# Performance work log

Measured on AMD Instinct MI355X. Metric: run time of the kernel, lower is better.

Reference implementation:

```python
import jax, jax.numpy as jnp
import numpy as np

N_AE = 64
N_GRAPHS = 4096
N_ELE = 16384
EPS = 1e-5


def _seg_mean(v, idx, num_segments):
    s = jax.ops.segment_sum(v, idx, num_segments=num_segments)
    c = jax.ops.segment_sum(jnp.ones((v.shape[0], 1), v.dtype), idx, num_segments=num_segments)
    return s / jnp.maximum(c, 1.0)


def _batchnorm(h, gamma, beta):
    mu = jnp.mean(h, axis=0)
    var = jnp.mean(jnp.square(h - mu), axis=0)  # biased, as torch BN training fwd
    return (h - mu) * jax.lax.rsqrt(var + EPS) * gamma + beta


def _dist_layer(x, dist_feat, atom_idx, ele_idx, W, b, gamma, beta):
    # x: [N, 2*n_ae]
    pa = jax.nn.relu(_seg_mean(x[:, :N_AE], atom_idx, N_GRAPHS))[atom_idx]   # [N, n_ae]
    pe = jax.nn.relu(_seg_mean(x[:, N_AE:], ele_idx, N_ELE))[ele_idx]        # [N, n_ae]
    h = jnp.concatenate([dist_feat, pa, pe], axis=1)                          # [N, n_de+2*n_ae]
    h = h @ W.T + b                                                           # [N, 2*n_ae]
    h = _batchnorm(h, gamma, beta)
    return jax.nn.relu(h + x)


def setup_inputs() -> dict:
    key = jax.random.key(0)
    ks = jax.random.split(key, 12)
    N = 500000
    n_re = 64
    n_be = 64
    d = 2 * N_AE
    inp = {
        "x": jax.random.normal(ks[0], (N, d), jnp.float32),
        "rdf_feat": jax.random.normal(ks[1], (N, n_re), jnp.float32),
        "bdf_feat": jax.random.normal(ks[2], (N, n_be), jnp.float32),
        "atom_idx": jnp.sort(jax.random.randint(ks[3], (N,), 0, N_GRAPHS)),
        "ele_idx": jax.random.randint(ks[4], (N,), 0, N_ELE),
        "rdf_W": jax.random.normal(ks[5], (d, n_re + d), jnp.float32) * 0.05,
        "rdf_b": jnp.zeros((d,), jnp.float32),
        "rdf_gamma": jnp.ones((d,), jnp.float32),
        "rdf_beta": jnp.zeros((d,), jnp.float32),
        "bdf_W": jax.random.normal(ks[6], (d, n_be + d), jnp.float32) * 0.05,
        "bdf_b": jnp.zeros((d,), jnp.float32),
        "bdf_gamma": jnp.ones((d,), jnp.float32),
        "bdf_beta": jnp.zeros((d,), jnp.float32),
        "fc_W": jax.random.normal(ks[7], (d, 2 * d), jnp.float32) * 0.05,
        "fc_b": jnp.zeros((d,), jnp.float32),
    }
    return inp


def reference(x, rdf_feat, bdf_feat, atom_idx, ele_idx,
              rdf_W, rdf_b, rdf_gamma, rdf_beta,
              bdf_W, bdf_b, bdf_gamma, bdf_beta,
              fc_W, fc_b):
    x1 = _dist_layer(x, rdf_feat, atom_idx, ele_idx, rdf_W, rdf_b, rdf_gamma, rdf_beta)
    x2 = _dist_layer(x, bdf_feat, atom_idx, ele_idx, bdf_W, bdf_b, bdf_gamma, bdf_beta)
    h = jnp.concatenate([x1, x2], axis=1)  # [N, 4*n_ae]
    return jax.nn.relu(h @ fc_W.T + fc_b)  # [N, 2*n_ae]
```

## Files before the change

kernel.cpp:

```cpp
#include <hip/hip_runtime.h>
#include <hip/hip_bf16.h>

#define N_GRAPHS 4096
#define N_ELE 16384
#define EPS 1e-5f

#define A_TAB_OFF 0
#define A_CNT_OFF 262144
#define E_TAB_OFF 266240
#define E_CNT_OFF 1314816
#define STAT_OFF  1331200
#define ZPAD_OFF  1347584
#define ZERO_WORDS 1347588
#define A_TABH_OFF 1347600
#define E_TABH_OFF 1478672
#define W1PK_OFF  2002960
#define FCPK_OFF  2027536
#define SCALE_OFF 2043920
#define SHIFT_OFF 2044176
#define WS_WORDS  2044432

typedef __attribute__((ext_vector_type(8))) short bf16x8;
typedef __attribute__((ext_vector_type(4))) float f32x4;

__device__ __forceinline__ float bf2f(unsigned s) { return __uint_as_float(s << 16); }
__device__ __forceinline__ unsigned f2bf(float f) {
  unsigned u = __float_as_uint(f);
  return (u + 0x7fffu + ((u >> 16) & 1u)) >> 16;
}
__device__ __forceinline__ unsigned pkbf(float a, float b) {
  union { __hip_bfloat16 h; unsigned short u; } ca, cb;
  ca.h = __float2bfloat16(a); cb.h = __float2bfloat16(b);
  return (unsigned)ca.u | ((unsigned)cb.u << 16);
}
__device__ __forceinline__ void gload16(const void* g, void* l) {
  __builtin_amdgcn_global_load_lds(
      (const __attribute__((address_space(1))) unsigned*)g,
      (__attribute__((address_space(3))) unsigned*)l, 16, 0, 0);
}


__global__ void k_prep(const float* __restrict__ W1, const float* __restrict__ W2,
                       const float* __restrict__ fcW, float* __restrict__ ws) {
  int tid = blockIdx.x * 512 + threadIdx.x;
  if (tid < 49152) {
    unsigned short* wpk = (unsigned short*)(ws + W1PK_OFF);
    int L = tid / 24576, rem = tid % 24576;
    int ct = rem / 3072, rem2 = rem % 3072;
    int i = rem2 >> 9, lane = (rem2 >> 3) & 63, j = rem2 & 7;
    int zkb = L ? (i + 2) : (i < 2 ? i : i + 2);
    int zk = zkb * 32 + ((lane >> 4) << 3) + j;
    int kp = L ? (zk - 64) : (zk < 64 ? zk : zk - 64);
    int col = ct * 16 + (lane & 15);
    const float* W = L ? W2 : W1;
    wpk[tid] = (unsigned short)f2bf(W[col * 192 + kp]);
  } else {
    int idx = tid - 49152;
    unsigned short* fpk = (unsigned short*)(ws + FCPK_OFF);
    int ct = idx >> 12, kb = (idx >> 9) & 7, lane = (idx >> 3) & 63, j = idx & 7;
    fpk[idx] = (unsigned short)f2bf(fcW[(ct * 16 + (lane & 15)) * 256 + kb * 32 + ((lane >> 4) << 3) + j]);
  }
}

__global__ void k_seg(const float* __restrict__ x, const int* __restrict__ aidx,
                      const int* __restrict__ eidx, float* __restrict__ ws, int N) {
  float* A_tab = ws + A_TAB_OFF; float* A_cnt = ws + A_CNT_OFF;
  float* E_tab = ws + E_TAB_OFF; float* E_cnt = ws + E_CNT_OFF;
  int t = threadIdx.x;
  int c = t & 63, p = (t >> 6) & 1, s = t >> 7;
  int r0 = blockIdx.x * 256;
  int rend = min(r0 + 256, N);
  if (p == 0) {
    float acc = 0.f, cnt = 0.f; int cur = -1;
    for (int r = r0 + s; r < rend; r += 2) {
      int a = aidx[r];
      float v = x[(size_t)r * 128 + c];
      if (a != cur) {
        if (cur >= 0) { atomicAdd(&A_tab[cur * 64 + c], acc); if (c == 0) atomicAdd(&A_cnt[cur], cnt); }
        cur = a; acc = v; cnt = 1.f;
      } else { acc += v; cnt += 1.f; }
    }
    if (cur >= 0) { atomicAdd(&A_tab[cur * 64 + c], acc); if (c == 0) atomicAdd(&A_cnt[cur], cnt); }
  } else {
    for (int r = r0 + s; r < rend; r += 2) {
      int e = eidx[r];
      float v = x[(size_t)r * 128 + 64 + c];
      atomicAdd(&E_tab[e * 64 + c], v);
      if (c == 0) atomicAdd(&E_cnt[e], 1.f);
    }
  }
}

__global__ void k_fin(float* __restrict__ ws) {
  int i = blockIdx.x * 256 + threadIdx.x;
  unsigned* w32 = (unsigned*)ws;
  if (i < 131072) {
    int e = 2 * i;
    float cnt = fmaxf(ws[A_CNT_OFF + (e >> 6)], 1.f);
    float v0 = fmaxf(ws[A_TAB_OFF + e] / cnt, 0.f);
    float v1 = fmaxf(ws[A_TAB_OFF + e + 1] / cnt, 0.f);
    w32[A_TABH_OFF + i] = f2bf(v0) | (f2bf(v1) << 16);
  }
  if (i < 524288) {
    int e = 2 * i;
    float cnt = fmaxf(ws[E_CNT_OFF + (e >> 6)], 1.f);
    float v0 = fmaxf(ws[E_TAB_OFF + e] / cnt, 0.f);
    float v1 = fmaxf(ws[E_TAB_OFF + e + 1] / cnt, 0.f);
    w32[E_TABH_OFF + i] = f2bf(v0) | (f2bf(v1) << 16);
  }
}

__global__ __launch_bounds__(512) void k_gemm(
    const float* __restrict__ rdf, const float* __restrict__ bdf,
    const int* __restrict__ aidx, const int* __restrict__ eidx,
    float* __restrict__ ws, unsigned* __restrict__ outp, int N) {
  __shared__ __align__(16) char smem[32768];
  const unsigned short* Atabh = (const unsigned short*)(ws + A_TABH_OFF);
  const unsigned short* Etabh = (const unsigned short*)(ws + E_TABH_OFF);
  const void* zpad = (const void*)(ws + ZPAD_OFF);
  int t = threadIdx.x;
  int l = t & 63, w = t >> 6;
  int row0 = blockIdx.x * 64;

  #pragma unroll
  for (int ii = 0; ii < 2; ++ii) {
    int rb = (w * 2 + ii) * 4;
    int r = rb + (l >> 4);
    int srow = row0 + r;
    bool ok = srow < N;
    int s = l & 15;
    int c = (s & 8) | ((s ^ r) & 7);
    const void* src;
    if (c < 8) {
      int ia = ok ? aidx[srow] : 0;
      src = (const void*)(Atabh + ((size_t)ia * 64 + c * 8));
    } else {
      int ie = ok ? eidx[srow] : 0;
      src = (const void*)(Etabh + ((size_t)ie * 64 + (c - 8) * 8));
    }
    if (!ok) src = zpad;
    gload16(src, smem + 16384 + rb * 256);
  }

  {
    int r = t >> 3, c0 = (t & 7) * 2;
    int row = row0 + r;
    bool ok = row < N;
    #pragma unroll
    for (int cc = 0; cc < 2; ++cc) {
      int c = c0 + cc;
      uint4 wv;
      if (ok) {
        const float4* src = (const float4*)(c < 8 ? rdf + (size_t)row * 64 + c * 8
                                                  : bdf + (size_t)row * 64 + (c - 8) * 8);
        float4 f0 = src[0], f1 = src[1];
        wv.x = pkbf(f0.x, f0.y); wv.y = pkbf(f0.z, f0.w);
        wv.z = pkbf(f1.x, f1.y); wv.w = pkbf(f1.z, f1.w);
      } else wv = (uint4){0u, 0u, 0u, 0u};
      int slot = (c & 8) | ((c ^ r) & 7);
      *(uint4*)(smem + r * 256 + slot * 16) = wv;
    }
  }
  __syncthreads();

  int L = w >> 2, ctp = w & 3;
  const unsigned short* WpkL = (const unsigned short*)(ws + W1PK_OFF) + L * 24576;
  f32x4 acc[4][2];
  #pragma unroll
  for (int mt = 0; mt < 4; ++mt)
    #pragma unroll
    for (int cti = 0; cti < 2; ++cti) acc[mt][cti] = (f32x4){0.f, 0.f, 0.f, 0.f};
  int half = l >> 4;
  #pragma unroll
  for (int i = 0; i < 6; ++i) {
    int zkb = L ? (i + 2) : (i < 2 ? i : i + 2);
    int cg = zkb * 4 + half;
    const char* base = smem + (zkb < 4 ? 0 : 16384);
    int cl = cg & 15;
    bf16x8 af[4];
    #pragma unroll
    for (int mt = 0; mt < 4; ++mt) {
      int rr = mt * 16 + (l & 15);
      int slot = (cl & 8) | ((cl ^ rr) & 7);
      af[mt] = *(const bf16x8*)(base + rr * 256 + slot * 16);
    }
    #pragma unroll
    for (int cti = 0; cti < 2; ++cti) {
      bf16x8 bfr = *(const bf16x8*)(WpkL + (((ctp * 2 + cti) * 6 + i) * 64 + l) * 8);
      #pragma unroll
      for (int mt = 0; mt < 4; ++mt)
        acc[mt][cti] = __builtin_amdgcn_mfma_f32_16x16x32_bf16(af[mt], bfr, acc[mt][cti], 0, 0, 0);
    }
  }

  float* stat = ws + STAT_OFF + (blockIdx.x & 31) * 512;
  #pragma unroll
  for (int cti = 0; cti < 2; ++cti) {
    float s = 0.f, q = 0.f;
    #pragma unroll
    for (int mt = 0; mt < 4; ++mt)
      #pragma unroll
      for (int rr = 0; rr < 4; ++rr) { float v = acc[mt][cti][rr]; s += v; q += v * v; }
    s += __shfl_xor(s, 16); s += __shfl_xor(s, 32);
    q += __shfl_xor(q, 16); q += __shfl_xor(q, 32);
    if (l < 16) {
      int gc = L * 128 + ctp * 32 + cti * 16 + l;
      atomicAdd(&stat[gc], s);
      atomicAdd(&stat[256 + gc], q);
    }
  }
  __syncthreads();

  #pragma unroll
  for (int mt = 0; mt < 4; ++mt)
    #pragma unroll
    for (int cti = 0; cti < 2; ++cti)
      #pragma unroll
      for (int rr = 0; rr < 4; ++rr) {
        unsigned ub = pkbf(acc[mt][cti][rr], 0.f) & 0xffffu;
        unsigned pb = (unsigned)__shfl_xor((int)ub, 1);
        if (!(l & 1)) {
          int orow = mt * 16 + ((l >> 4) << 2) + rr;
          int colp = (L * 128 + ctp * 32 + cti * 16 + (l & 15)) >> 1;
          int c = colp >> 2;
          int ec = ((c ^ orow) & 7) | (c & 24);
          *(unsigned*)(smem + orow * 512 + ec * 16 + (colp & 3) * 4) = ub | (pb << 16);
        }
      }
  __syncthreads();
  #pragma unroll
  for (int p = 0; p < 4; ++p) {
    int e = p * 512 + t; int rr = e >> 5, v4 = e & 31;
    int ec = ((v4 ^ rr) & 7) | (v4 & 24);
    uint4 val = *(const uint4*)(smem + rr * 512 + ec * 16);
    if (row0 + rr < N) ((uint4*)outp)[(size_t)(row0 + rr) * 32 + v4] = val;
  }
}

__global__ void k_bnfin(const float* __restrict__ g1, const float* __restrict__ b1,
                        const float* __restrict__ g2, const float* __restrict__ b2,
                        float* __restrict__ ws, int N) {
  int c = threadIdx.x;
  float s = 0.f, q = 0.f;
  for (int m = 0; m < 32; ++m) { s += ws[STAT_OFF + m * 512 + c]; q += ws[STAT_OFF + m * 512 + 256 + c]; }
  float inv = 1.f / (float)N;
  float mu = s * inv;
  float var = fmaxf(q * inv - mu * mu, 0.f);
  int lyr = c >> 7, cc = c & 127;
  float ga = lyr ? g2[cc] : g1[cc];
  float be = lyr ? b2[cc] : b1[cc];
  float sc = ga * rsqrtf(var + EPS);
  ws[SCALE_OFF + c] = sc;
  ws[SHIFT_OFF + c] = be - mu * sc;
}

__global__ __launch_bounds__(512) void k_fc(
    const float* __restrict__ x, const float* __restrict__ fcb,
    float* __restrict__ ws, float* __restrict__ out, int N) {
  __shared__ __align__(16) char smem[32768];
  __shared__ float scsh[512];
  int t = threadIdx.x;
  int l = t & 63, w = t >> 6;
  int r = t >> 3, g = t & 7;
  const unsigned* hp = (const unsigned*)out;
  int row0 = blockIdx.x * 64;
  int row = row0 + r;
  bool ok = row < N;
  uint4 hv[4]; float4 xv[8];
  if (ok) {
    const uint4* hs = (const uint4*)(hp + (size_t)row * 128 + g * 16);
    #pragma unroll
    for (int i = 0; i < 4; ++i) hv[i] = hs[i];
    const float4* xs = (const float4*)(x + (size_t)row * 128 + (g & 3) * 32);
    #pragma unroll
    for (int i = 0; i < 8; ++i) xv[i] = xs[i];
  } else {
    #pragma unroll
    for (int i = 0; i < 4; ++i) hv[i] = (uint4){0u, 0u, 0u, 0u};
    #pragma unroll
    for (int i = 0; i < 8; ++i) xv[i] = (float4){0.f, 0.f, 0.f, 0.f};
  }
  scsh[t] = ws[SCALE_OFF + t];
  __syncthreads();
  {
    unsigned wv[16];
    const unsigned* hu = (const unsigned*)hv;
    const float* xf = (const float*)xv;
    #pragma unroll
    for (int j = 0; j < 16; ++j) {
      int c = g * 32 + 2 * j;
      float lo = bf2f(hu[j] & 0xffffu) * scsh[c]     + scsh[256 + c]     + xf[2 * j];
      float hi = bf2f(hu[j] >> 16)     * scsh[c + 1] + scsh[256 + c + 1] + xf[2 * j + 1];
      wv[j] = pkbf(fmaxf(lo, 0.f), fmaxf(hi, 0.f));
    }
    #pragma unroll
    for (int i = 0; i < 4; ++i) {
      int slot = ((g ^ r ^ i) & 7) | (i << 3);
      *(uint4*)(smem + r * 512 + slot * 16) = ((uint4*)wv)[i];
    }
  }
  __syncthreads();
  f32x4 acc[4];
  #pragma unroll
  for (int mt = 0; mt < 4; ++mt) acc[mt] = (f32x4){0.f, 0.f, 0.f, 0.f};
  const unsigned short* Fpk = (const unsigned short*)(ws + FCPK_OFF);
  int half = l >> 4;
  #pragma unroll
  for (int kb = 0; kb < 8; ++kb) {
    bf16x8 bfr = *(const bf16x8*)(Fpk + ((w * 8 + kb) * 64 + l) * 8);
    #pragma unroll
    for (int mt = 0; mt < 4; ++mt) {
      int rr = mt * 16 + (l & 15);
      int slot = ((kb ^ rr ^ half) & 7) | (half << 3);
      bf16x8 af = *(const bf16x8*)(smem + rr * 512 + slot * 16);
      acc[mt] = __builtin_amdgcn_mfma_f32_16x16x32_bf16(af, bfr, acc[mt], 0, 0, 0);
    }
  }
  float bias = fcb[(w << 4) + (l & 15)];
  __syncthreads();
  #pragma unroll
  for (int mt = 0; mt < 4; ++mt)
    #pragma unroll
    for (int rr = 0; rr < 4; ++rr) {
      int orow = mt * 16 + ((l >> 4) << 2) + rr;
      int col = (w << 4) + (l & 15);
      int c = col >> 2;
      int ec = ((c ^ orow) & 7) | (c & 24);
      *(float*)(smem + orow * 512 + ec * 16 + (col & 3) * 4) = fmaxf(acc[mt][rr] + bias, 0.f);
    }
  __syncthreads();
  #pragma unroll
  for (int p = 0; p < 4; ++p) {
    int e = p * 512 + t; int rr = e >> 5, v4 = e & 31;
    int ec = ((v4 ^ rr) & 7) | (v4 & 24);
    float4 val = *(const float4*)(smem + rr * 512 + ec * 16);
    if (row0 + rr < N) ((float4*)out)[(size_t)(row0 + rr) * 32 + v4] = val;
  }
}

extern "C" void kernel_launch(void* const* d_in, const int* in_sizes, int n_in,
                              void* d_out, int out_size, void* d_ws, size_t ws_size,
                              hipStream_t stream) {
  const float* x    = (const float*)d_in[0];
  const float* rdf  = (const float*)d_in[1];
  const float* bdf  = (const float*)d_in[2];
  const int*   aidx = (const int*)d_in[3];
  const int*   eidx = (const int*)d_in[4];
  const float* rdfW = (const float*)d_in[5];
  const float* rdfG = (const float*)d_in[7];
  const float* rdfBe= (const float*)d_in[8];
  const float* bdfW = (const float*)d_in[9];
  const float* bdfG = (const float*)d_in[11];
  const float* bdfBe= (const float*)d_in[12];
  const float* fcW  = (const float*)d_in[13];
  const float* fcB  = (const float*)d_in[14];
  float* out = (float*)d_out;
  float* ws  = (float*)d_ws;
  int N = in_sizes[0] / 128;
  int nT = (N + 63) / 64;

  hipMemsetAsync(d_ws, 0, (size_t)ZERO_WORDS * 4, stream);
  k_prep<<<160, 512, 0, stream>>>(rdfW, bdfW, fcW, ws);
  k_seg<<<(N + 255) / 256, 256, 0, stream>>>(x, aidx, eidx, ws, N);
  k_fin<<<2048, 256, 0, stream>>>(ws);
  k_gemm<<<nT, 512, 0, stream>>>(rdf, bdf, aidx, eidx, ws, (unsigned*)d_out, N);
  k_bnfin<<<1, 256, 0, stream>>>(rdfG, rdfBe, bdfG, bdfBe, ws, N);
  k_fc<<<nT, 512, 0, stream>>>(x, fcB, ws, out, N);
}
```

Baseline: 482.9 us.

## Give each wave full-width 16-row tiles with register A operands in both GEMMs

Both GEMM kernels are restructured so each wave owns 16 rows and computes all output columns. A fragments are loaded straight from global memory into registers, which removes the shared-memory staging of inputs and the block-wide barriers. The weight packing order is changed to match the new fragment indexing. In k_gemm, BN statistics are reduced per block in shared memory first, so only one atomic per column per block is issued. The cost is many more accumulator registers per thread and more redundant global weight fragment reads, with 256-thread blocks replacing 512-thread ones.

```diff
diff --git a/kernel.cpp b/kernel.cpp
--- a/kernel.cpp
+++ b/kernel.cpp
@@ -33,31 +33,30 @@
   ca.h = __float2bfloat16(a); cb.h = __float2bfloat16(b);
   return (unsigned)ca.u | ((unsigned)cb.u << 16);
 }
-__device__ __forceinline__ void gload16(const void* g, void* l) {
-  __builtin_amdgcn_global_load_lds(
-      (const __attribute__((address_space(1))) unsigned*)g,
-      (__attribute__((address_space(3))) unsigned*)l, 16, 0, 0);
-}
-
+__device__ __forceinline__ bf16x8 cvt8(float4 a, float4 b) {
+  union { bf16x8 v; unsigned u[4]; } r;
+  r.u[0] = pkbf(a.x, a.y); r.u[1] = pkbf(a.z, a.w);
+  r.u[2] = pkbf(b.x, b.y); r.u[3] = pkbf(b.z, b.w);
+  return r.v;
+}
 
 __global__ void k_prep(const float* __restrict__ W1, const float* __restrict__ W2,
                        const float* __restrict__ fcW, float* __restrict__ ws) {
   int tid = blockIdx.x * 512 + threadIdx.x;
   if (tid < 49152) {
     unsigned short* wpk = (unsigned short*)(ws + W1PK_OFF);
-    int L = tid / 24576, rem = tid % 24576;
-    int ct = rem / 3072, rem2 = rem % 3072;
-    int i = rem2 >> 9, lane = (rem2 >> 3) & 63, j = rem2 & 7;
-    int zkb = L ? (i + 2) : (i < 2 ? i : i + 2);
-    int zk = zkb * 32 + ((lane >> 4) << 3) + j;
-    int kp = L ? (zk - 64) : (zk < 64 ? zk : zk - 64);
-    int col = ct * 16 + (lane & 15);
+    int ord = tid >> 9, lane = (tid >> 3) & 63, j = tid & 7;
+    int zkb, L, ct;
+    if (ord < 32) { zkb = ord >> 3; L = (zkb >= 2); ct = ord & 7; }
+    else { int o = ord - 32; zkb = 4 + (o >> 4); L = (o >> 3) & 1; ct = o & 7; }
+    int kW = (zkb - (zkb >= 2 ? 2 : 0)) * 32 + ((lane >> 4) << 3) + j;
     const float* W = L ? W2 : W1;
-    wpk[tid] = (unsigned short)f2bf(W[col * 192 + kp]);
+    wpk[tid] = (unsigned short)f2bf(W[(ct * 16 + (lane & 15)) * 192 + kW]);
   } else {
     int idx = tid - 49152;
     unsigned short* fpk = (unsigned short*)(ws + FCPK_OFF);
-    int ct = idx >> 12, kb = (idx >> 9) & 7, lane = (idx >> 3) & 63, j = idx & 7;
+    int ord = idx >> 9, lane = (idx >> 3) & 63, j = idx & 7;
+    int kb = ord >> 3, ct = ord & 7;
     fpk[idx] = (unsigned short)f2bf(fcW[(ct * 16 + (lane & 15)) * 256 + kb * 32 + ((lane >> 4) << 3) + j]);
   }
 }
@@ -110,130 +109,95 @@
   }
 }
 
-__global__ __launch_bounds__(512) void k_gemm(
+#define MM8(A, ACC, S) { _Pragma("unroll") \
+  for (int ct = 0; ct < 8; ++ct) ACC[ct] = __builtin_amdgcn_mfma_f32_16x16x32_bf16(A, Bp[(S + ct) * 64], ACC[ct], 0, 0, 0); }
+
+__global__ __launch_bounds__(256) void k_gemm(
     const float* __restrict__ rdf, const float* __restrict__ bdf,
     const int* __restrict__ aidx, const int* __restrict__ eidx,
     float* __restrict__ ws, unsigned* __restrict__ outp, int N) {
-  __shared__ __align__(16) char smem[32768];
+  __shared__ __align__(16) char smem[40960];
   const unsigned short* Atabh = (const unsigned short*)(ws + A_TABH_OFF);
   const unsigned short* Etabh = (const unsigned short*)(ws + E_TABH_OFF);
-  const void* zpad = (const void*)(ws + ZPAD_OFF);
-  int t = threadIdx.x;
-  int l = t & 63, w = t >> 6;
-  int row0 = blockIdx.x * 64;
-
-  #pragma unroll
-  for (int ii = 0; ii < 2; ++ii) {
-    int rb = (w * 2 + ii) * 4;
-    int r = rb + (l >> 4);
-    int srow = row0 + r;
-    bool ok = srow < N;
-    int s = l & 15;
-    int c = (s & 8) | ((s ^ r) & 7);
-    const void* src;
-    if (c < 8) {
-      int ia = ok ? aidx[srow] : 0;
-      src = (const void*)(Atabh + ((size_t)ia * 64 + c * 8));
-    } else {
-      int ie = ok ? eidx[srow] : 0;
-      src = (const void*)(Etabh + ((size_t)ie * 64 + (c - 8) * 8));
-    }
-    if (!ok) src = zpad;
-    gload16(src, smem + 16384 + rb * 256);
-  }
-
-  {
-    int r = t >> 3, c0 = (t & 7) * 2;
-    int row = row0 + r;
-    bool ok = row < N;
-    #pragma unroll
-    for (int cc = 0; cc < 2; ++cc) {
-      int c = c0 + cc;
-      uint4 wv;
-      if (ok) {
-        const float4* src = (const float4*)(c < 8 ? rdf + (size_t)row * 64 + c * 8
-                                                  : bdf + (size_t)row * 64 + (c - 8) * 8);
-        float4 f0 = src[0], f1 = src[1];
-        wv.x = pkbf(f0.x, f0.y); wv.y = pkbf(f0.z, f0.w);
-        wv.z = pkbf(f1.x, f1.y); wv.w = pkbf(f1.z, f1.w);
-      } else wv = (uint4){0u, 0u, 0u, 0u};
-      int slot = (c & 8) | ((c ^ r) & 7);
-      *(uint4*)(smem + r * 256 + slot * 16) = wv;
-    }
-  }
+  int t = threadIdx.x, l = t & 63, w = t >> 6;
+  int row0 = blockIdx.x * 64 + w * 16;
+  int row = row0 + (l & 15);
+  bool ok = row < N;
+  int rowc = ok ? row : 0;
+  int koff = (l >> 4) << 3;
+
+  int ia = aidx[rowc], ie = eidx[rowc];
+  const float* r0 = rdf + (size_t)rowc * 64 + koff;
+  const float* b0 = bdf + (size_t)rowc * 64 + koff;
+  bf16x8 a0 = cvt8(*(const float4*)r0, *(const float4*)(r0 + 4));
+  bf16x8 a1 = cvt8(*(const float4*)(r0 + 32), *(const float4*)(r0 + 36));
+  bf16x8 a2 = cvt8(*(const float4*)b0, *(const float4*)(b0 + 4));
+  bf16x8 a3 = cvt8(*(const float4*)(b0 + 32), *(const float4*)(b0 + 36));
+  const char* pa = (const char*)(Atabh + (size_t)ia * 64 + koff);
+  const char* pe = (const char*)(Etabh + (size_t)ie * 64 + koff);
+  bf16x8 a4 = *(const bf16x8*)pa;
+  bf16x8 a5 = *(const bf16x8*)(pa + 64);
+  bf16x8 a6 = *(const bf16x8*)pe;
+  bf16x8 a7 = *(const bf16x8*)(pe + 64);
+  if (!ok) {
+    bf16x8 z = (bf16x8){0,0,0,0,0,0,0,0};
+    a0 = z; a1 = z; a2 = z; a3 = z; a4 = z; a5 = z; a6 = z; a7 = z;
+  }
+
+  const bf16x8* Bp = (const bf16x8*)((const unsigned short*)(ws + W1PK_OFF) + (size_t)l * 8);
+  f32x4 acc0[8], acc1[8];
+  #pragma unroll
+  for (int ct = 0; ct < 8; ++ct) { acc0[ct] = (f32x4){0.f,0.f,0.f,0.f}; acc1[ct] = (f32x4){0.f,0.f,0.f,0.f}; }
+  MM8(a0, acc0, 0)  MM8(a1, acc0, 8)
+  MM8(a2, acc1, 16) MM8(a3, acc1, 24)
+  MM8(a4, acc0, 32) MM8(a4, acc1, 40)
+  MM8(a5, acc0, 48) MM8(a5, acc1, 56)
+  MM8(a6, acc0, 64) MM8(a6, acc1, 72)
+  MM8(a7, acc0, 80) MM8(a7, acc1, 88)
+
+  float* statf = (float*)(smem + 32768);
+  #define STAT8(ACC, L) { _Pragma("unroll") for (int ct = 0; ct < 8; ++ct) { \
+    f32x4 A_ = ACC[ct]; \
+    float s_ = A_[0] + A_[1] + A_[2] + A_[3]; \
+    float q_ = A_[0]*A_[0] + A_[1]*A_[1] + A_[2]*A_[2] + A_[3]*A_[3]; \
+    s_ += __shfl_xor(s_, 16); s_ += __shfl_xor(s_, 32); \
+    q_ += __shfl_xor(q_, 16); q_ += __shfl_xor(q_, 32); \
+    if (l < 16) { int gc = L * 128 + ct * 16 + l; \
+      statf[w * 512 + gc] = s_; statf[w * 512 + 256 + gc] = q_; } } }
+  STAT8(acc0, 0)
+  STAT8(acc1, 1)
+
+  char* T = smem + w * 8192;
+  #define TWR(ACC, L) { _Pragma("unroll") for (int ct = 0; ct < 8; ++ct) { \
+    _Pragma("unroll") for (int rr = 0; rr < 4; ++rr) { \
+      unsigned ub = pkbf(ACC[ct][rr], 0.f) & 0xffffu; \
+      unsigned pb = (unsigned)__shfl_xor((int)ub, 1); \
+      if (!(l & 1)) { \
+        int rowt = ((l >> 4) << 2) + rr; \
+        int gc = L * 128 + ct * 16 + (l & 15); \
+        int ch = gc >> 3; \
+        int cs = (ch & 24) | ((ch ^ rowt) & 7); \
+        *(unsigned*)(T + rowt * 512 + cs * 16 + ((gc >> 1) & 3) * 4) = ub | (pb << 16); } } } }
+  TWR(acc0, 0)
+  TWR(acc1, 1)
+  asm volatile("s_waitcnt lgkmcnt(0)" ::: "memory");
+  __builtin_amdgcn_sched_barrier(0);
+  #pragma unroll
+  for (int q = 0; q < 8; ++q) {
+    int rowt = l >> 2, cl = ((l & 3) << 3) + q;
+    int cs = (cl & 24) | ((cl ^ rowt) & 7);
+    uint4 v = *(const uint4*)(T + rowt * 512 + cs * 16);
+    int grow = row0 + rowt;
+    if (grow < N) *(uint4*)((char*)outp + (size_t)grow * 512 + cl * 16) = v;
+  }
+
   __syncthreads();
-
-  int L = w >> 2, ctp = w & 3;
-  const unsigned short* WpkL = (const unsigned short*)(ws + W1PK_OFF) + L * 24576;
-  f32x4 acc[4][2];
-  #pragma unroll
-  for (int mt = 0; mt < 4; ++mt)
-    #pragma unroll
-    for (int cti = 0; cti < 2; ++cti) acc[mt][cti] = (f32x4){0.f, 0.f, 0.f, 0.f};
-  int half = l >> 4;
-  #pragma unroll
-  for (int i = 0; i < 6; ++i) {
-    int zkb = L ? (i + 2) : (i < 2 ? i : i + 2);
-    int cg = zkb * 4 + half;
-    const char* base = smem + (zkb < 4 ? 0 : 16384);
-    int cl = cg & 15;
-    bf16x8 af[4];
-    #pragma unroll
-    for (int mt = 0; mt < 4; ++mt) {
-      int rr = mt * 16 + (l & 15);
-      int slot = (cl & 8) | ((cl ^ rr) & 7);
-      af[mt] = *(const bf16x8*)(base + rr * 256 + slot * 16);
-    }
-    #pragma unroll
-    for (int cti = 0; cti < 2; ++cti) {
-      bf16x8 bfr = *(const bf16x8*)(WpkL + (((ctp * 2 + cti) * 6 + i) * 64 + l) * 8);
-      #pragma unroll
-      for (int mt = 0; mt < 4; ++mt)
-        acc[mt][cti] = __builtin_amdgcn_mfma_f32_16x16x32_bf16(af[mt], bfr, acc[mt][cti], 0, 0, 0);
-    }
-  }
-
   float* stat = ws + STAT_OFF + (blockIdx.x & 31) * 512;
   #pragma unroll
-  for (int cti = 0; cti < 2; ++cti) {
-    float s = 0.f, q = 0.f;
-    #pragma unroll
-    for (int mt = 0; mt < 4; ++mt)
-      #pragma unroll
-      for (int rr = 0; rr < 4; ++rr) { float v = acc[mt][cti][rr]; s += v; q += v * v; }
-    s += __shfl_xor(s, 16); s += __shfl_xor(s, 32);
-    q += __shfl_xor(q, 16); q += __shfl_xor(q, 32);
-    if (l < 16) {
-      int gc = L * 128 + ctp * 32 + cti * 16 + l;
-      atomicAdd(&stat[gc], s);
-      atomicAdd(&stat[256 + gc], q);
-    }
-  }
-  __syncthreads();
-
-  #pragma unroll
-  for (int mt = 0; mt < 4; ++mt)
-    #pragma unroll
-    for (int cti = 0; cti < 2; ++cti)
-      #pragma unroll
-      for (int rr = 0; rr < 4; ++rr) {
-        unsigned ub = pkbf(acc[mt][cti][rr], 0.f) & 0xffffu;
-        unsigned pb = (unsigned)__shfl_xor((int)ub, 1);
-        if (!(l & 1)) {
-          int orow = mt * 16 + ((l >> 4) << 2) + rr;
-          int colp = (L * 128 + ctp * 32 + cti * 16 + (l & 15)) >> 1;
-          int c = colp >> 2;
-          int ec = ((c ^ orow) & 7) | (c & 24);
-          *(unsigned*)(smem + orow * 512 + ec * 16 + (colp & 3) * 4) = ub | (pb << 16);
-        }
-      }
-  __syncthreads();
-  #pragma unroll
-  for (int p = 0; p < 4; ++p) {
-    int e = p * 512 + t; int rr = e >> 5, v4 = e & 31;
-    int ec = ((v4 ^ rr) & 7) | (v4 & 24);
-    uint4 val = *(const uint4*)(smem + rr * 512 + ec * 16);
-    if (row0 + rr < N) ((uint4*)outp)[(size_t)(row0 + rr) * 32 + v4] = val;
+  for (int u = 0; u < 2; ++u) {
+    int c = t + u * 256;
+    float r = statf[c] + statf[512 + c] + statf[1024 + c] + statf[1536 + c];
+    atomicAdd(&stat[c], r);
   }
 }
 
@@ -254,87 +218,70 @@
   ws[SHIFT_OFF + c] = be - mu * sc;
 }
 
-__global__ __launch_bounds__(512) void k_fc(
+__global__ __launch_bounds__(256) void k_fc(
     const float* __restrict__ x, const float* __restrict__ fcb,
     float* __restrict__ ws, float* __restrict__ out, int N) {
   __shared__ __align__(16) char smem[32768];
-  __shared__ float scsh[512];
-  int t = threadIdx.x;
-  int l = t & 63, w = t >> 6;
-  int r = t >> 3, g = t & 7;
-  const unsigned* hp = (const unsigned*)out;
-  int row0 = blockIdx.x * 64;
-  int row = row0 + r;
+  int t = threadIdx.x, l = t & 63, w = t >> 6;
+  int row0 = blockIdx.x * 64 + w * 16;
+  int row = row0 + (l & 15);
   bool ok = row < N;
-  uint4 hv[4]; float4 xv[8];
-  if (ok) {
-    const uint4* hs = (const uint4*)(hp + (size_t)row * 128 + g * 16);
+  int rowc = ok ? row : 0;
+  int koff = (l >> 4) << 3;
+  const char* hp = (const char*)out;
+  const bf16x8* Bp = (const bf16x8*)((const unsigned short*)(ws + FCPK_OFF) + (size_t)l * 8);
+  f32x4 acc[8];
+  #pragma unroll
+  for (int ct = 0; ct < 8; ++ct) acc[ct] = (f32x4){0.f,0.f,0.f,0.f};
+
+  #pragma unroll
+  for (int kb = 0; kb < 8; ++kb) {
+    int k0 = kb * 32 + koff;
+    uint4 hr = *(const uint4*)(hp + (size_t)rowc * 512 + k0 * 2);
+    const float* xb = x + (size_t)rowc * 128 + (k0 & 127);
+    const float* scp = ws + SCALE_OFF + k0;
+    const float* shp = ws + SHIFT_OFF + k0;
+    float xs[8], sc[8], sh[8];
+    ((float4*)xs)[0] = *(const float4*)xb;       ((float4*)xs)[1] = *(const float4*)(xb + 4);
+    ((float4*)sc)[0] = *(const float4*)scp;      ((float4*)sc)[1] = *(const float4*)(scp + 4);
+    ((float4*)sh)[0] = *(const float4*)shp;      ((float4*)sh)[1] = *(const float4*)(shp + 4);
+    const unsigned* hu = (const unsigned*)&hr;
+    union { bf16x8 v; unsigned u[4]; } A_;
     #pragma unroll
-    for (int i = 0; i < 4; ++i) hv[i] = hs[i];
-    const float4* xs = (const float4*)(x + (size_t)row * 128 + (g & 3) * 32);
+    for (int j = 0; j < 4; ++j) {
+      float lo = bf2f(hu[j] & 0xffffu) * sc[2*j]     + sh[2*j]     + xs[2*j];
+      float hi = bf2f(hu[j] >> 16)     * sc[2*j + 1] + sh[2*j + 1] + xs[2*j + 1];
+      A_.u[j] = pkbf(fmaxf(lo, 0.f), fmaxf(hi, 0.f));
+    }
+    bf16x8 A = A_.v;
+    if (!ok) A = (bf16x8){0,0,0,0,0,0,0,0};
     #pragma unroll
-    for (int i = 0; i < 8; ++i) xv[i] = xs[i];
-  } else {
-    #pragma unroll
-    for (int i = 0; i < 4; ++i) hv[i] = (uint4){0u, 0u, 0u, 0u};
-    #pragma unroll
-    for (int i = 0; i < 8; ++i) xv[i] = (float4){0.f, 0.f, 0.f, 0.f};
-  }
-  scsh[t] = ws[SCALE_OFF + t];
-  __syncthreads();
-  {
-    unsigned wv[16];
-    const unsigned* hu = (const unsigned*)hv;
-    const float* xf = (const float*)xv;
-    #pragma unroll
-    for (int j = 0; j < 16; ++j) {
-      int c = g * 32 + 2 * j;
-      float lo = bf2f(hu[j] & 0xffffu) * scsh[c]     + scsh[256 + c]     + xf[2 * j];
-      float hi = bf2f(hu[j] >> 16)     * scsh[c + 1] + scsh[256 + c + 1] + xf[2 * j + 1];
-      wv[j] = pkbf(fmaxf(lo, 0.f), fmaxf(hi, 0.f));
-    }
-    #pragma unroll
-    for (int i = 0; i < 4; ++i) {
-      int slot = ((g ^ r ^ i) & 7) | (i << 3);
-      *(uint4*)(smem + r * 512 + slot * 16) = ((uint4*)wv)[i];
-    }
-  }
-  __syncthreads();
-  f32x4 acc[4];
-  #pragma unroll
-  for (int mt = 0; mt < 4; ++mt) acc[mt] = (f32x4){0.f, 0.f, 0.f, 0.f};
-  const unsigned short* Fpk = (const unsigned short*)(ws + FCPK_OFF);
-  int half = l >> 4;
-  #pragma unroll
-  for (int kb = 0; kb < 8; ++kb) {
-    bf16x8 bfr = *(const bf16x8*)(Fpk + ((w * 8 + kb) * 64 + l) * 8);
-    #pragma unroll
-    for (int mt = 0; mt < 4; ++mt) {
-      int rr = mt * 16 + (l & 15);
-      int slot = ((kb ^ rr ^ half) & 7) | (half << 3);
-      bf16x8 af = *(const bf16x8*)(smem + rr * 512 + slot * 16);
-      acc[mt] = __builtin_amdgcn_mfma_f32_16x16x32_bf16(af, bfr, acc[mt], 0, 0, 0);
-    }
-  }
-  float bias = fcb[(w << 4) + (l & 15)];
-  __syncthreads();
-  #pragma unroll
-  for (int mt = 0; mt < 4; ++mt)
+    for (int ct = 0; ct < 8; ++ct)
+      acc[ct] = __builtin_amdgcn_mfma_f32_16x16x32_bf16(A, Bp[(kb * 8 + ct) * 64], acc[ct], 0, 0, 0);
+  }
+
+  char* T = smem + w * 8192;
+  #pragma unroll
+  for (int ct = 0; ct < 8; ++ct) {
+    float bias = fcb[ct * 16 + (l & 15)];
     #pragma unroll
     for (int rr = 0; rr < 4; ++rr) {
-      int orow = mt * 16 + ((l >> 4) << 2) + rr;
-      int col = (w << 4) + (l & 15);
-      int c = col >> 2;
-      int ec = ((c ^ orow) & 7) | (c & 24);
-      *(float*)(smem + orow * 512 + ec * 16 + (col & 3) * 4) = fmaxf(acc[mt][rr] + bias, 0.f);
+      int rowt = ((l >> 4) << 2) + rr;
+      int col = ct * 16 + (l & 15);
+      int ch = col >> 2;
+      int cs = (ch & 24) | ((ch ^ rowt) & 7);
+      *(float*)(T + rowt * 512 + cs * 16 + (col & 3) * 4) = fmaxf(acc[ct][rr] + bias, 0.f);
     }
-  __syncthreads();
-  #pragma unroll
-  for (int p = 0; p < 4; ++p) {
-    int e = p * 512 + t; int rr = e >> 5, v4 = e & 31;
-    int ec = ((v4 ^ rr) & 7) | (v4 & 24);
-    float4 val = *(const float4*)(smem + rr * 512 + ec * 16);
-    if (row0 + rr < N) ((float4*)out)[(size_t)(row0 + rr) * 32 + v4] = val;
+  }
+  asm volatile("s_waitcnt lgkmcnt(0)" ::: "memory");
+  __builtin_amdgcn_sched_barrier(0);
+  #pragma unroll
+  for (int q = 0; q < 8; ++q) {
+    int rowt = l >> 2, cl = ((l & 3) << 3) + q;
+    int cs = (cl & 24) | ((cl ^ rowt) & 7);
+    float4 v = *(const float4*)(T + rowt * 512 + cs * 16);
+    int grow = row0 + rowt;
+    if (grow < N) *(float4*)(out + (size_t)grow * 128 + cl * 4) = v;
   }
 }
 
@@ -363,7 +310,7 @@
   k_prep<<<160, 512, 0, stream>>>(rdfW, bdfW, fcW, ws);
   k_seg<<<(N + 255) / 256, 256, 0, stream>>>(x, aidx, eidx, ws, N);
   k_fin<<<2048, 256, 0, stream>>>(ws);
-  k_gemm<<<nT, 512, 0, stream>>>(rdf, bdf, aidx, eidx, ws, (unsigned*)d_out, N);
+  k_gemm<<<nT, 256, 0, stream>>>(rdf, bdf, aidx, eidx, ws, (unsigned*)d_out, N);
   k_bnfin<<<1, 256, 0, stream>>>(rdfG, rdfBe, bdfG, bdfBe, ws, N);
-  k_fc<<<nT, 512, 0, stream>>>(x, fcB, ws, out, N);
-}
+  k_fc<<<nT, 256, 0, stream>>>(x, fcB, ws, out, N);
+}
```

Result: slower. 903.4 us (+87.1%).

## Process multiple tiles per block with double-buffered prefetch in gemm and fc kernels

Applied to the files above, without the earlier changes.

Both the distance-layer GEMM and the final FC kernel now handle four 64-row tiles per block. They use two LDS buffers so the next tile's gathered tables and features are loaded while the current tile runs on MFMA. MFMA sections are wrapped in s_setprio, and the fc kernel's load/column mapping is rearranged so each thread reads 16 x columns instead of 32. The aim is to hide global and gather latency and amortise per-block setup. In exchange LDS doubles to 64KB, which lowers occupancy, and the grid shrinks fourfold, which could leave CUs underfilled.

```diff
diff --git a/kernel.cpp b/kernel.cpp
--- a/kernel.cpp
+++ b/kernel.cpp
@@ -4,6 +4,7 @@
 #define N_GRAPHS 4096
 #define N_ELE 16384
 #define EPS 1e-5f
+#define TPB 4
 
 #define A_TAB_OFF 0
 #define A_CNT_OFF 262144
@@ -38,7 +39,6 @@
       (const __attribute__((address_space(1))) unsigned*)g,
       (__attribute__((address_space(3))) unsigned*)l, 16, 0, 0);
 }
-
 
 __global__ void k_prep(const float* __restrict__ W1, const float* __restrict__ W2,
                        const float* __restrict__ fcW, float* __restrict__ ws) {
@@ -110,18 +110,10 @@
   }
 }
 
-__global__ __launch_bounds__(512) void k_gemm(
-    const float* __restrict__ rdf, const float* __restrict__ bdf,
+__device__ __forceinline__ void stage_zb(const unsigned short* __restrict__ Atabh,
+    const unsigned short* __restrict__ Etabh, const void* zpad,
     const int* __restrict__ aidx, const int* __restrict__ eidx,
-    float* __restrict__ ws, unsigned* __restrict__ outp, int N) {
-  __shared__ __align__(16) char smem[32768];
-  const unsigned short* Atabh = (const unsigned short*)(ws + A_TABH_OFF);
-  const unsigned short* Etabh = (const unsigned short*)(ws + E_TABH_OFF);
-  const void* zpad = (const void*)(ws + ZPAD_OFF);
-  int t = threadIdx.x;
-  int l = t & 63, w = t >> 6;
-  int row0 = blockIdx.x * 64;
-
+    int row0, int w, int l, char* zb, int N) {
   #pragma unroll
   for (int ii = 0; ii < 2; ++ii) {
     int rb = (w * 2 + ii) * 4;
@@ -131,109 +123,152 @@
     int s = l & 15;
     int c = (s & 8) | ((s ^ r) & 7);
     const void* src;
-    if (c < 8) {
-      int ia = ok ? aidx[srow] : 0;
-      src = (const void*)(Atabh + ((size_t)ia * 64 + c * 8));
+    if (c < 8) { int ia = ok ? aidx[srow] : 0; src = (const void*)(Atabh + ((size_t)ia * 64 + c * 8)); }
+    else       { int ie = ok ? eidx[srow] : 0; src = (const void*)(Etabh + ((size_t)ie * 64 + (c - 8) * 8)); }
+    if (!ok) src = zpad;
+    gload16(src, zb + rb * 256);
+  }
+}
+
+__device__ __forceinline__ void load_za(const float* __restrict__ rdf, const float* __restrict__ bdf,
+    int row0, int t, float4* fv, int N) {
+  int r = t >> 3, c0 = (t & 7) * 2;
+  int row = row0 + r;
+  bool ok = row < N;
+  #pragma unroll
+  for (int cc = 0; cc < 2; ++cc) {
+    int c = c0 + cc;
+    if (ok) {
+      const float4* src = (const float4*)(c < 8 ? rdf + (size_t)row * 64 + c * 8
+                                                : bdf + (size_t)row * 64 + (c - 8) * 8);
+      fv[cc * 2] = src[0]; fv[cc * 2 + 1] = src[1];
     } else {
-      int ie = ok ? eidx[srow] : 0;
-      src = (const void*)(Etabh + ((size_t)ie * 64 + (c - 8) * 8));
-    }
-    if (!ok) src = zpad;
-    gload16(src, smem + 16384 + rb * 256);
-  }
-
-  {
-    int r = t >> 3, c0 = (t & 7) * 2;
-    int row = row0 + r;
-    bool ok = row < N;
-    #pragma unroll
-    for (int cc = 0; cc < 2; ++cc) {
-      int c = c0 + cc;
-      uint4 wv;
-      if (ok) {
-        const float4* src = (const float4*)(c < 8 ? rdf + (size_t)row * 64 + c * 8
-                                                  : bdf + (size_t)row * 64 + (c - 8) * 8);
-        float4 f0 = src[0], f1 = src[1];
-        wv.x = pkbf(f0.x, f0.y); wv.y = pkbf(f0.z, f0.w);
-        wv.z = pkbf(f1.x, f1.y); wv.w = pkbf(f1.z, f1.w);
-      } else wv = (uint4){0u, 0u, 0u, 0u};
-      int slot = (c & 8) | ((c ^ r) & 7);
-      *(uint4*)(smem + r * 256 + slot * 16) = wv;
-    }
-  }
+      fv[cc * 2] = (float4){0.f, 0.f, 0.f, 0.f};
+      fv[cc * 2 + 1] = (float4){0.f, 0.f, 0.f, 0.f};
+    }
+  }
+}
+
+__device__ __forceinline__ void cvt_za(const float4* fv, int t, char* za) {
+  int r = t >> 3, c0 = (t & 7) * 2;
+  #pragma unroll
+  for (int cc = 0; cc < 2; ++cc) {
+    int c = c0 + cc;
+    uint4 wv;
+    wv.x = pkbf(fv[cc * 2].x, fv[cc * 2].y);     wv.y = pkbf(fv[cc * 2].z, fv[cc * 2].w);
+    wv.z = pkbf(fv[cc * 2 + 1].x, fv[cc * 2 + 1].y); wv.w = pkbf(fv[cc * 2 + 1].z, fv[cc * 2 + 1].w);
+    int slot = (c & 8) | ((c ^ r) & 7);
+    *(uint4*)(za + r * 256 + slot * 16) = wv;
+  }
+}
+
+__global__ __launch_bounds__(512) void k_gemm(
+    const float* __restrict__ rdf, const float* __restrict__ bdf,
+    const int* __restrict__ aidx, const int* __restrict__ eidx,
+    float* __restrict__ ws, unsigned* __restrict__ outp, int N, int nT) {
+  __shared__ __align__(16) char smem[65536];
+  const unsigned short* Atabh = (const unsigned short*)(ws + A_TABH_OFF);
+  const unsigned short* Etabh = (const unsigned short*)(ws + E_TABH_OFF);
+  const void* zpad = (const void*)(ws + ZPAD_OFF);
+  int t = threadIdx.x;
+  int l = t & 63, w = t >> 6;
+  int L = w >> 2, ctp = w & 3;
+  int half = l >> 4;
+  const unsigned short* WpkL = (const unsigned short*)(ws + W1PK_OFF) + L * 24576;
+  float* stat = ws + STAT_OFF + (blockIdx.x & 31) * 512;
+  int tile0 = blockIdx.x * TPB;
+  float4 fv[4];
+
+  stage_zb(Atabh, Etabh, zpad, aidx, eidx, tile0 * 64, w, l, smem + 16384, N);
+  load_za(rdf, bdf, tile0 * 64, t, fv, N);
+  cvt_za(fv, t, smem);
   __syncthreads();
 
-  int L = w >> 2, ctp = w & 3;
-  const unsigned short* WpkL = (const unsigned short*)(ws + W1PK_OFF) + L * 24576;
-  f32x4 acc[4][2];
-  #pragma unroll
-  for (int mt = 0; mt < 4; ++mt)
-    #pragma unroll
-    for (int cti = 0; cti < 2; ++cti) acc[mt][cti] = (f32x4){0.f, 0.f, 0.f, 0.f};
-  int half = l >> 4;
-  #pragma unroll
-  for (int i = 0; i < 6; ++i) {
-    int zkb = L ? (i + 2) : (i < 2 ? i : i + 2);
-    int cg = zkb * 4 + half;
-    const char* base = smem + (zkb < 4 ? 0 : 16384);
-    int cl = cg & 15;
-    bf16x8 af[4];
-    #pragma unroll
-    for (int mt = 0; mt < 4; ++mt) {
-      int rr = mt * 16 + (l & 15);
-      int slot = (cl & 8) | ((cl ^ rr) & 7);
-      af[mt] = *(const bf16x8*)(base + rr * 256 + slot * 16);
-    }
+  for (int j = 0; j < TPB; ++j) {
+    int tile = tile0 + j;
+    if (tile >= nT) break;
+    int cur = j & 1;
+    char* bufC = smem + cur * 32768;
+    char* bufN = smem + (cur ^ 1) * 32768;
+    bool hasN = (j + 1 < TPB) && (tile + 1 < nT);
+    if (hasN) {
+      stage_zb(Atabh, Etabh, zpad, aidx, eidx, (tile + 1) * 64, w, l, bufN + 16384, N);
+      load_za(rdf, bdf, (tile + 1) * 64, t, fv, N);
+    }
+
+    f32x4 acc[4][2];
+    #pragma unroll
+    for (int mt = 0; mt < 4; ++mt)
+      #pragma unroll
+      for (int cti = 0; cti < 2; ++cti) acc[mt][cti] = (f32x4){0.f, 0.f, 0.f, 0.f};
+    __builtin_amdgcn_s_setprio(1);
+    #pragma unroll
+    for (int i = 0; i < 6; ++i) {
+      int zkb = L ? (i + 2) : (i < 2 ? i : i + 2);
+      int cg = zkb * 4 + half;
+      const char* base = bufC + (zkb < 4 ? 0 : 16384);
+      int cl = cg & 15;
+      bf16x8 af[4];
+      #pragma unroll
+      for (int mt = 0; mt < 4; ++mt) {
+        int rr = mt * 16 + (l & 15);
+        int slot = (cl & 8) | ((cl ^ rr) & 7);
+        af[mt] = *(const bf16x8*)(base + rr * 256 + slot * 16);
+      }
+      #pragma unroll
+      for (int cti = 0; cti < 2; ++cti) {
+        bf16x8 bfr = *(const bf16x8*)(WpkL + (((ctp * 2 + cti) * 6 + i) * 64 + l) * 8);
+        #pragma unroll
+        for (int mt = 0; mt < 4; ++mt)
+          acc[mt][cti] = __builtin_amdgcn_mfma_f32_16x16x32_bf16(af[mt], bfr, acc[mt][cti], 0, 0, 0);
+      }
+    }
+    __builtin_amdgcn_s_setprio(0);
+
     #pragma unroll
     for (int cti = 0; cti < 2; ++cti) {
-      bf16x8 bfr = *(const bf16x8*)(WpkL + (((ctp * 2 + cti) * 6 + i) * 64 + l) * 8);
+      float s = 0.f, q = 0.f;
       #pragma unroll
       for (int mt = 0; mt < 4; ++mt)
-        acc[mt][cti] = __builtin_amdgcn_mfma_f32_16x16x32_bf16(af[mt], bfr, acc[mt][cti], 0, 0, 0);
-    }
-  }
-
-  float* stat = ws + STAT_OFF + (blockIdx.x & 31) * 512;
-  #pragma unroll
-  for (int cti = 0; cti < 2; ++cti) {
-    float s = 0.f, q = 0.f;
+        #pragma unroll
+        for (int rr = 0; rr < 4; ++rr) { float v = acc[mt][cti][rr]; s += v; q += v * v; }
+      s += __shfl_xor(s, 16); s += __shfl_xor(s, 32);
+      q += __shfl_xor(q, 16); q += __shfl_xor(q, 32);
+      if (l < 16) {
+        int gc = L * 128 + (ctp * 2 + cti) * 16 + l;
+        atomicAdd(&stat[gc], s);
+        atomicAdd(&stat[256 + gc], q);
+      }
+    }
+    __syncthreads();
+
     #pragma unroll
     for (int mt = 0; mt < 4; ++mt)
       #pragma unroll
-      for (int rr = 0; rr < 4; ++rr) { float v = acc[mt][cti][rr]; s += v; q += v * v; }
-    s += __shfl_xor(s, 16); s += __shfl_xor(s, 32);
-    q += __shfl_xor(q, 16); q += __shfl_xor(q, 32);
-    if (l < 16) {
-      int gc = L * 128 + ctp * 32 + cti * 16 + l;
-      atomicAdd(&stat[gc], s);
-      atomicAdd(&stat[256 + gc], q);
-    }
-  }
-  __syncthreads();
-
-  #pragma unroll
-  for (int mt = 0; mt < 4; ++mt)
-    #pragma unroll
-    for (int cti = 0; cti < 2; ++cti)
-      #pragma unroll
-      for (int rr = 0; rr < 4; ++rr) {
-        unsigned ub = pkbf(acc[mt][cti][rr], 0.f) & 0xffffu;
-        unsigned pb = (unsigned)__shfl_xor((int)ub, 1);
-        if (!(l & 1)) {
-          int orow = mt * 16 + ((l >> 4) << 2) + rr;
-          int colp = (L * 128 + ctp * 32 + cti * 16 + (l & 15)) >> 1;
-          int c = colp >> 2;
-          int ec = ((c ^ orow) & 7) | (c & 24);
-          *(unsigned*)(smem + orow * 512 + ec * 16 + (colp & 3) * 4) = ub | (pb << 16);
+      for (int cti = 0; cti < 2; ++cti)
+        #pragma unroll
+        for (int rr = 0; rr < 4; ++rr) {
+          unsigned ub = pkbf(acc[mt][cti][rr], 0.f) & 0xffffu;
+          unsigned pb = (unsigned)__shfl_xor((int)ub, 1);
+          if (!(l & 1)) {
+            int orow = mt * 16 + ((l >> 4) << 2) + rr;
+            int colp = (L * 128 + (ctp * 2 + cti) * 16 + (l & 15)) >> 1;
+            int ch = colp >> 2;
+            int cs = ((ch ^ orow) & 7) | (ch & 24);
+            *(unsigned*)(bufC + orow * 512 + cs * 16 + (colp & 3) * 4) = ub | (pb << 16);
+          }
         }
-      }
-  __syncthreads();
-  #pragma unroll
-  for (int p = 0; p < 4; ++p) {
-    int e = p * 512 + t; int rr = e >> 5, v4 = e & 31;
-    int ec = ((v4 ^ rr) & 7) | (v4 & 24);
-    uint4 val = *(const uint4*)(smem + rr * 512 + ec * 16);
-    if (row0 + rr < N) ((uint4*)outp)[(size_t)(row0 + rr) * 32 + v4] = val;
+    __syncthreads();
+    int row0 = tile * 64;
+    #pragma unroll
+    for (int p = 0; p < 4; ++p) {
+      int e = p * 512 + t; int rr = e >> 5, v4 = e & 31;
+      int cs = ((v4 ^ rr) & 7) | (v4 & 24);
+      uint4 val = *(const uint4*)(bufC + rr * 512 + cs * 16);
+      if (row0 + rr < N) ((uint4*)outp)[(size_t)(row0 + rr) * 32 + v4] = val;
+    }
+    if (hasN) cvt_za(fv, t, bufN);
+    __syncthreads();
   }
 }
 
@@ -254,87 +289,116 @@
   ws[SHIFT_OFF + c] = be - mu * sc;
 }
 
+__device__ __forceinline__ void load_fc(const unsigned* __restrict__ hp, const float* __restrict__ x,
+    int row0, int t, uint4* hv, float4* xv, int N) {
+  int r = t >> 3, g = t & 7;
+  int row = row0 + r;
+  if (row < N) {
+    const uint4* hs = (const uint4*)((const char*)hp + (size_t)row * 512);
+    hv[0] = hs[2 * g]; hv[1] = hs[2 * g + 1]; hv[2] = hs[2 * g + 16]; hv[3] = hs[2 * g + 17];
+    const float4* xs = (const float4*)(x + (size_t)row * 128 + g * 16);
+    xv[0] = xs[0]; xv[1] = xs[1]; xv[2] = xs[2]; xv[3] = xs[3];
+  } else {
+    #pragma unroll
+    for (int i = 0; i < 4; ++i) { hv[i] = (uint4){0u,0u,0u,0u}; xv[i] = (float4){0.f,0.f,0.f,0.f}; }
+  }
+}
+
+__device__ __forceinline__ void proc_fc(const uint4* hv, const float4* xv, const float* scsh,
+    int t, char* z) {
+  int r = t >> 3, g = t & 7;
+  const unsigned* hu = (const unsigned*)hv;
+  const float* xf = (const float*)xv;
+  #pragma unroll
+  for (int hh = 0; hh < 2; ++hh) {
+    #pragma unroll
+    for (int d = 0; d < 2; ++d) {
+      uint4 wq;
+      unsigned* wu = (unsigned*)&wq;
+      #pragma unroll
+      for (int jj = 0; jj < 4; ++jj) {
+        int xi = d * 8 + 2 * jj;
+        int k = g * 16 + hh * 128 + d * 8 + 2 * jj;
+        unsigned hraw = hu[hh * 8 + d * 4 + jj];
+        float lo = bf2f(hraw & 0xffffu) * scsh[k]     + scsh[256 + k]     + xf[xi];
+        float hi = bf2f(hraw >> 16)     * scsh[k + 1] + scsh[256 + k + 1] + xf[xi + 1];
+        wu[jj] = pkbf(fmaxf(lo, 0.f), fmaxf(hi, 0.f));
+      }
+      int c = 2 * g + hh * 16 + d;
+      int kb = c >> 2, hf = c & 3;
+      int slot = (hf << 3) | ((kb ^ r ^ hf) & 7);
+      *(uint4*)(z + r * 512 + slot * 16) = wq;
+    }
+  }
+}
+
 __global__ __launch_bounds__(512) void k_fc(
     const float* __restrict__ x, const float* __restrict__ fcb,
-    float* __restrict__ ws, float* __restrict__ out, int N) {
-  __shared__ __align__(16) char smem[32768];
+    float* __restrict__ ws, float* __restrict__ out, int N, int nT) {
+  __shared__ __align__(16) char smem[65536];
   __shared__ float scsh[512];
-  int t = threadIdx.x;
-  int l = t & 63, w = t >> 6;
-  int r = t >> 3, g = t & 7;
+  int t = threadIdx.x, l = t & 63, w = t >> 6;
   const unsigned* hp = (const unsigned*)out;
-  int row0 = blockIdx.x * 64;
-  int row = row0 + r;
-  bool ok = row < N;
-  uint4 hv[4]; float4 xv[8];
-  if (ok) {
-    const uint4* hs = (const uint4*)(hp + (size_t)row * 128 + g * 16);
-    #pragma unroll
-    for (int i = 0; i < 4; ++i) hv[i] = hs[i];
-    const float4* xs = (const float4*)(x + (size_t)row * 128 + (g & 3) * 32);
-    #pragma unroll
-    for (int i = 0; i < 8; ++i) xv[i] = xs[i];
-  } else {
-    #pragma unroll
-    for (int i = 0; i < 4; ++i) hv[i] = (uint4){0u, 0u, 0u, 0u};
-    #pragma unroll
-    for (int i = 0; i < 8; ++i) xv[i] = (float4){0.f, 0.f, 0.f, 0.f};
-  }
-  scsh[t] = ws[SCALE_OFF + t];
-  __syncthreads();
-  {
-    unsigned wv[16];
-    const unsigned* hu = (const unsigned*)hv;
-    const float* xf = (const float*)xv;
-    #pragma unroll
-    for (int j = 0; j < 16; ++j) {
-      int c = g * 32 + 2 * j;
-      float lo = bf2f(hu[j] & 0xffffu) * scsh[c]     + scsh[256 + c]     + xf[2 * j];
-      float hi = bf2f(hu[j] >> 16)     * scsh[c + 1] + scsh[256 + c + 1] + xf[2 * j + 1];
-      wv[j] = pkbf(fmaxf(lo, 0.f), fmaxf(hi, 0.f));
-    }
-    #pragma unroll
-    for (int i = 0; i < 4; ++i) {
-      int slot = ((g ^ r ^ i) & 7) | (i << 3);
-      *(uint4*)(smem + r * 512 + slot * 16) = ((uint4*)wv)[i];
-    }
-  }
-  __syncthreads();
-  f32x4 acc[4];
-  #pragma unroll
-  for (int mt = 0; mt < 4; ++mt) acc[mt] = (f32x4){0.f, 0.f, 0.f, 0.f};
   const unsigned short* Fpk = (const unsigned short*)(ws + FCPK_OFF);
   int half = l >> 4;
-  #pragma unroll
-  for (int kb = 0; kb < 8; ++kb) {
-    bf16x8 bfr = *(const bf16x8*)(Fpk + ((w * 8 + kb) * 64 + l) * 8);
-    #pragma unroll
-    for (int mt = 0; mt < 4; ++mt) {
-      int rr = mt * 16 + (l & 15);
-      int slot = ((kb ^ rr ^ half) & 7) | (half << 3);
-      bf16x8 af = *(const bf16x8*)(smem + rr * 512 + slot * 16);
-      acc[mt] = __builtin_amdgcn_mfma_f32_16x16x32_bf16(af, bfr, acc[mt], 0, 0, 0);
-    }
-  }
+  int tile0 = blockIdx.x * TPB;
+  uint4 hv[4]; float4 xv[4];
+
+  scsh[t] = ws[SCALE_OFF + t];
+  load_fc(hp, x, tile0 * 64, t, hv, xv, N);
   float bias = fcb[(w << 4) + (l & 15)];
   __syncthreads();
-  #pragma unroll
-  for (int mt = 0; mt < 4; ++mt)
-    #pragma unroll
-    for (int rr = 0; rr < 4; ++rr) {
-      int orow = mt * 16 + ((l >> 4) << 2) + rr;
-      int col = (w << 4) + (l & 15);
-      int c = col >> 2;
-      int ec = ((c ^ orow) & 7) | (c & 24);
-      *(float*)(smem + orow * 512 + ec * 16 + (col & 3) * 4) = fmaxf(acc[mt][rr] + bias, 0.f);
-    }
+  proc_fc(hv, xv, scsh, t, smem);
   __syncthreads();
-  #pragma unroll
-  for (int p = 0; p < 4; ++p) {
-    int e = p * 512 + t; int rr = e >> 5, v4 = e & 31;
-    int ec = ((v4 ^ rr) & 7) | (v4 & 24);
-    float4 val = *(const float4*)(smem + rr * 512 + ec * 16);
-    if (row0 + rr < N) ((float4*)out)[(size_t)(row0 + rr) * 32 + v4] = val;
+
+  for (int j = 0; j < TPB; ++j) {
+    int tile = tile0 + j;
+    if (tile >= nT) break;
+    int cur = j & 1;
+    char* bufC = smem + cur * 32768;
+    char* bufN = smem + (cur ^ 1) * 32768;
+    bool hasN = (j + 1 < TPB) && (tile + 1 < nT);
+    if (hasN) load_fc(hp, x, (tile + 1) * 64, t, hv, xv, N);
+
+    f32x4 acc[4];
+    #pragma unroll
+    for (int mt = 0; mt < 4; ++mt) acc[mt] = (f32x4){0.f, 0.f, 0.f, 0.f};
+    __builtin_amdgcn_s_setprio(1);
+    #pragma unroll
+    for (int kb = 0; kb < 8; ++kb) {
+      bf16x8 bfr = *(const bf16x8*)(Fpk + ((w * 8 + kb) * 64 + l) * 8);
+      #pragma unroll
+      for (int mt = 0; mt < 4; ++mt) {
+        int rr = mt * 16 + (l & 15);
+        int slot = ((kb ^ rr ^ half) & 7) | (half << 3);
+        bf16x8 af = *(const bf16x8*)(bufC + rr * 512 + slot * 16);
+        acc[mt] = __builtin_amdgcn_mfma_f32_16x16x32_bf16(af, bfr, acc[mt], 0, 0, 0);
+      }
+    }
+    __builtin_amdgcn_s_setprio(0);
+    __syncthreads();
+
+    #pragma unroll
+    for (int mt = 0; mt < 4; ++mt)
+      #pragma unroll
+      for (int rr = 0; rr < 4; ++rr) {
+        int orow = mt * 16 + ((l >> 4) << 2) + rr;
+        int col = (w << 4) + (l & 15);
+        int ch = col >> 2;
+        int cs = ((ch ^ orow) & 7) | (ch & 24);
+        *(float*)(bufC + orow * 512 + cs * 16 + (col & 3) * 4) = fmaxf(acc[mt][rr] + bias, 0.f);
+      }
+    __syncthreads();
+    int row0 = tile * 64;
+    #pragma unroll
+    for (int p = 0; p < 4; ++p) {
+      int e = p * 512 + t; int rr = e >> 5, v4 = e & 31;
+      int cs = ((v4 ^ rr) & 7) | (v4 & 24);
+      float4 val = *(const float4*)(bufC + rr * 512 + cs * 16);
+      if (row0 + rr < N) ((float4*)out)[(size_t)(row0 + rr) * 32 + v4] = val;
+    }
+    if (hasN) proc_fc(hv, xv, scsh, t, bufN);
+    __syncthreads();
   }
 }
 
@@ -358,12 +422,13 @@
   float* ws  = (float*)d_ws;
   int N = in_sizes[0] / 128;
   int nT = (N + 63) / 64;
+  int gridP = (nT + TPB - 1) / TPB;
 
   hipMemsetAsync(d_ws, 0, (size_t)ZERO_WORDS * 4, stream);
   k_prep<<<160, 512, 0, stream>>>(rdfW, bdfW, fcW, ws);
   k_seg<<<(N + 255) / 256, 256, 0, stream>>>(x, aidx, eidx, ws, N);
   k_fin<<<2048, 256, 0, stream>>>(ws);
-  k_gemm<<<nT, 512, 0, stream>>>(rdf, bdf, aidx, eidx, ws, (unsigned*)d_out, N);
+  k_gemm<<<gridP, 512, 0, stream>>>(rdf, bdf, aidx, eidx, ws, (unsigned*)d_out, N, nT);
   k_bnfin<<<1, 256, 0, stream>>>(rdfG, rdfBe, bdfG, bdfBe, ws, N);
-  k_fc<<<nT, 512, 0, stream>>>(x, fcB, ws, out, N);
-}
+  k_fc<<<gridP, 512, 0, stream>>>(x, fcB, ws, out, N, nT);
+}
```

After: 558.7 us. 1.16x slower.
